# Kernel tuning notes

Measured on AMD Instinct MI355X. Metric: run time of the kernel, lower is better.

## Reference

```python
import jax, jax.numpy as jnp
import numpy as np

V = 32000   # vocab_size
HD = 512    # num_hiddens
B = 32      # batch
T = 128     # seq_len


def setup_inputs() -> dict:
    key = jax.random.key(0)
    ks = jax.random.split(key, 11)
    s_in = 1.0 / np.sqrt(V + HD)   # torch Linear default init bound
    s_out = 1.0 / np.sqrt(HD)

    def lin_w(k, out_f, in_f, s):
        return jax.random.uniform(k, (out_f, in_f), jnp.float32, -s, s)

    def lin_b(k, out_f, s):
        return jax.random.uniform(k, (out_f,), jnp.float32, -s, s)

    return {
        "X": jax.random.randint(ks[0], (B, T), 0, V),
        "H": jnp.zeros((B, HD), jnp.float32),
        "C": jnp.zeros((B, HD), jnp.float32),
        "Wf": lin_w(ks[1], HD, V + HD, s_in), "bf": lin_b(ks[2], HD, s_in),
        "Wi": lin_w(ks[3], HD, V + HD, s_in), "bi": lin_b(ks[4], HD, s_in),
        "Wo": lin_w(ks[5], HD, V + HD, s_in), "bo": lin_b(ks[6], HD, s_in),
        "Wc": lin_w(ks[7], HD, V + HD, s_in), "bc": lin_b(ks[8], HD, s_in),
        "Wy": lin_w(ks[9], V, HD, s_out),     "by": lin_b(ks[10], V, s_out),
    }


def reference(X, H, C, Wf, bf, Wi, bi, Wo, bo, Wc, bc, Wy, by):
    # X: [B, T] int tokens. Transposed to time-major like torch's X.T.
    Xt = X.T  # [T, B]
    hd = H.shape[1]
    v = Wf.shape[1] - hd

    def split(W):
        return W[:, :v], W[:, v:]  # input part, hidden part

    Wfx, Wfh = split(Wf)
    Wix, Wih = split(Wi)
    Wox, Woh = split(Wo)
    Wcx, Wch = split(Wc)

    # one_hot(x) @ Wx^T == row-gather of Wx^T: same math, no wasted compute.
    Ef = jnp.take(Wfx.T, Xt, axis=0) + bf  # [T, B, HD]
    Ei = jnp.take(Wix.T, Xt, axis=0) + bi
    Eo = jnp.take(Wox.T, Xt, axis=0) + bo
    Ec = jnp.take(Wcx.T, Xt, axis=0) + bc

    def step(carry, e):
        h, c = carry
        ef, ei, eo, ec = e
        f = jax.nn.sigmoid(ef + h @ Wfh.T)
        i = jax.nn.sigmoid(ei + h @ Wih.T)
        o = jax.nn.sigmoid(eo + h @ Woh.T)
        c_tilde = jnp.tanh(ec + h @ Wch.T)
        c = f * c + i * c_tilde
        h = o * jnp.tanh(c)
        return (h, c), h

    (H, C), Hs = jax.lax.scan(step, (H, C), (Ef, Ei, Eo, Ec))  # Hs: [T, B, HD]

    # per-step Y = h2out(H), then torch.cat(outputs, dim=0) -> [T*B, V]
    Y = Hs.reshape(-1, hd) @ Wy.T + by
    return Y, (H, C)
```

## Files before the change

### kernel.cpp

```cpp
#include <hip/hip_runtime.h>
#include <hip/hip_bf16.h>

#define V  32000
#define HD 512
#define BB 32
#define TT 128
#define VH 32512
#define LBLK 8
#define NBLK 256
#define GBLK (NBLK - LBLK)
#define NTILE (32 * 125)

typedef short  short8  __attribute__((ext_vector_type(8)));
typedef unsigned short u16x8 __attribute__((ext_vector_type(8)));
typedef unsigned short u16x4 __attribute__((ext_vector_type(4)));
typedef float  f32x4   __attribute__((ext_vector_type(4)));

__device__ __forceinline__ unsigned short bf16_rne(float f) {
  unsigned u = __builtin_bit_cast(unsigned, f);
  u += 0x7FFFu + ((u >> 16) & 1u);
  return (unsigned short)(u >> 16);
}

__device__ __forceinline__ void gload_lds16(const void* g, void* l) {
  __builtin_amdgcn_global_load_lds((const __attribute__((address_space(1))) void*)g,
                                   (__attribute__((address_space(3))) void*)l, 16, 0, 0);
}

__device__ __forceinline__ float sigf(float x) {
  return 1.0f / (1.0f + __expf(-x));
}
__device__ __forceinline__ float tanhf_fast(float x) {
  return 1.0f - 2.0f / (1.0f + __expf(2.0f * x));
}

__global__ void __launch_bounds__(512, 2) fused_all(
    const int* __restrict__ X,
    const float* __restrict__ Hin,
    const float* __restrict__ Cin,
    const float* __restrict__ Wf, const float* __restrict__ bfp,
    const float* __restrict__ Wi, const float* __restrict__ bip,
    const float* __restrict__ Wo, const float* __restrict__ bop,
    const float* __restrict__ Wc, const float* __restrict__ bcp,
    const float* __restrict__ Wy, const float* __restrict__ by,
    float* __restrict__ E,
    unsigned short* __restrict__ HsM1,
    unsigned short* __restrict__ Wyb,
    float* __restrict__ outHC,
    unsigned* __restrict__ bar,
    unsigned* __restrict__ bar2,
    unsigned* __restrict__ gcount,
    unsigned* __restrict__ wbar,
    float* __restrict__ Y)
{
  __shared__ __align__(16) char smem[75776];

  const int tid = threadIdx.x;
  const int blkid = blockIdx.x;
  const int wid = tid >> 6, lane = tid & 63;
  const int fr = lane & 15, ko = lane >> 4;

  unsigned short* Hs = HsM1 + BB * HD;

  if (blkid < LBLK) {
    short* hl = (short*)smem;
    float (*Pl)[BB][68] = (float(*)[BB][68])(smem + 32768);
    float (*cl)[64]     = (float(*)[64])(smem + 32768 + 34816);

    const int blk = blkid;
    const int g = wid & 3, qg = wid >> 2;

    const float* Wg = (g == 0) ? Wf : (g == 1) ? Wi : (g == 2) ? Wo : Wc;
    short8 wreg[2][16];
    #pragma unroll
    for (int n = 0; n < 2; ++n) {
      const int q = blk * 64 + qg * 32 + n * 16 + fr;
      const float* rowp = Wg + (size_t)q * VH + V;
      #pragma unroll
      for (int kk = 0; kk < 16; ++kk) {
        const float4 lo = *(const float4*)(rowp + kk * 32 + ko * 8);
        const float4 hi = *(const float4*)(rowp + kk * 32 + ko * 8 + 4);
        short8 w;
        w[0] = (short)bf16_rne(lo.x); w[1] = (short)bf16_rne(lo.y);
        w[2] = (short)bf16_rne(lo.z); w[3] = (short)bf16_rne(lo.w);
        w[4] = (short)bf16_rne(hi.x); w[5] = (short)bf16_rne(hi.y);
        w[6] = (short)bf16_rne(hi.z); w[7] = (short)bf16_rne(hi.w);
        wreg[n][kk] = w;
      }
    }

    const int e0 = tid * 4;
    const int eb = e0 >> 6, ql = e0 & 63;
    const int qglob = blk * 64 + ql;
    {
      const f32x4 c4 = *(const f32x4*)(Cin + eb * HD + qglob);
      *(f32x4*)&cl[eb][ql] = c4;
      const f32x4 h4 = *(const f32x4*)(Hin + eb * HD + qglob);
      u16x4 hq;
      #pragma unroll
      for (int j = 0; j < 4; ++j) hq[j] = bf16_rne(h4[j]);
      *(u16x4*)(HsM1 + (size_t)eb * HD + qglob) = hq;
    }
    __syncthreads();

    if (tid == 0) {
      __threadfence();
      __hip_atomic_fetch_add(bar, 1u, __ATOMIC_RELAXED, __HIP_MEMORY_SCOPE_AGENT);
      while (__hip_atomic_load(bar, __ATOMIC_RELAXED, __HIP_MEMORY_SCOPE_AGENT) < (unsigned)LBLK ||
             __hip_atomic_load(gcount, __ATOMIC_RELAXED, __HIP_MEMORY_SCOPE_AGENT) < (unsigned)TT) {}
      __threadfence();
    }
    __syncthreads();

    int abase[2], asw[2];
    #pragma unroll
    for (int m = 0; m < 2; ++m) {
      const int r = m * 16 + fr;
      abase[m] = r * 1024;
      asw[m] = (r & 7) << 4;
    }

    for (int t = 0; t < TT; ++t) {
      const float* Eb = E + ((size_t)t * 4) * BB * HD;
      const f32x4 ef = *(const f32x4*)(Eb + (size_t)(0 * BB + eb) * HD + qglob);
      const f32x4 ei = *(const f32x4*)(Eb + (size_t)(1 * BB + eb) * HD + qglob);
      const f32x4 eo = *(const f32x4*)(Eb + (size_t)(2 * BB + eb) * HD + qglob);
      const f32x4 ec = *(const f32x4*)(Eb + (size_t)(3 * BB + eb) * HD + qglob);

      if (t > 0) {
        __syncthreads();
        if (tid == 0) {
          __threadfence();
          __hip_atomic_fetch_add(bar, 1u, __ATOMIC_RELAXED, __HIP_MEMORY_SCOPE_AGENT);
          const unsigned tgt = (unsigned)(LBLK * (t + 1));
          while (__hip_atomic_load(bar, __ATOMIC_RELAXED, __HIP_MEMORY_SCOPE_AGENT) < tgt) {}
          __threadfence();
          if (blk == 0)
            __hip_atomic_store(bar2, (unsigned)t, __ATOMIC_RELAXED, __HIP_MEMORY_SCOPE_AGENT);
        }
        __syncthreads();
      }

      const char* hsrc = (const char*)(HsM1 + (size_t)t * (BB * HD));
      #pragma unroll
      for (int is = 0; is < 4; ++is) {
        const int i = is * 512 + tid;
        const int sb = (i >> 6) * 1024 + (((i & 63) * 16) ^ (((i >> 6) & 7) << 4));
        gload_lds16(hsrc + sb, (char*)hl + (size_t)(is * 512 + (tid & ~63)) * 16);
      }

      __syncthreads();

      f32x4 acc[2][2];
      #pragma unroll
      for (int m = 0; m < 2; ++m)
        #pragma unroll
        for (int n = 0; n < 2; ++n)
          acc[m][n] = (f32x4){0.f, 0.f, 0.f, 0.f};

      #pragma unroll
      for (int kk = 0; kk < 16; ++kk) {
        const int off = kk * 64 + ko * 16;
        const short8 a0 = *(const short8*)((const char*)hl + abase[0] + (off ^ asw[0]));
        const short8 a1 = *(const short8*)((const char*)hl + abase[1] + (off ^ asw[1]));
        acc[0][0] = __builtin_amdgcn_mfma_f32_16x16x32_bf16(a0, wreg[0][kk], acc[0][0], 0, 0, 0);
        acc[1][0] = __builtin_amdgcn_mfma_f32_16x16x32_bf16(a1, wreg[0][kk], acc[1][0], 0, 0, 0);
        acc[0][1] = __builtin_amdgcn_mfma_f32_16x16x32_bf16(a0, wreg[1][kk], acc[0][1], 0, 0, 0);
        acc[1][1] = __builtin_amdgcn_mfma_f32_16x16x32_bf16(a1, wreg[1][kk], acc[1][1], 0, 0, 0);
      }

      #pragma unroll
      for (int m = 0; m < 2; ++m)
        #pragma unroll
        for (int n = 0; n < 2; ++n)
          #pragma unroll
          for (int j = 0; j < 4; ++j)
            Pl[g][m * 16 + ko * 4 + j][qg * 32 + n * 16 + fr] = acc[m][n][j];
      __syncthreads();

      const f32x4 pf4 = *(const f32x4*)&Pl[0][eb][ql];
      const f32x4 pi4 = *(const f32x4*)&Pl[1][eb][ql];
      const f32x4 po4 = *(const f32x4*)&Pl[2][eb][ql];
      const f32x4 pc4 = *(const f32x4*)&Pl[3][eb][ql];
      const f32x4 cold = *(const f32x4*)&cl[eb][ql];
      f32x4 cnew, hnew;
      u16x4 hq;
      #pragma unroll
      for (int j = 0; j < 4; ++j) {
        const float fg = sigf(pf4[j] + ef[j]);
        const float ig = sigf(pi4[j] + ei[j]);
        const float og = sigf(po4[j] + eo[j]);
        const float ct = tanhf_fast(pc4[j] + ec[j]);
        const float cn = fg * cold[j] + ig * ct;
        const float hv = og * tanhf_fast(cn);
        cnew[j] = cn;
        hnew[j] = hv;
        hq[j] = bf16_rne(hv);
      }
      *(f32x4*)&cl[eb][ql] = cnew;
      *(u16x4*)(Hs + ((size_t)t * BB + eb) * HD + qglob) = hq;
      if (t == TT - 1) {
        *(f32x4*)(outHC + (size_t)eb * HD + qglob) = hnew;
        *(f32x4*)(outHC + (size_t)BB * HD + (size_t)eb * HD + qglob) = cnew;
      }
    }

    __syncthreads();
    if (tid == 0) {
      __threadfence();
      __hip_atomic_fetch_add(bar, 1u, __ATOMIC_RELAXED, __HIP_MEMORY_SCOPE_AGENT);
      if (blk == 0) {
        while (__hip_atomic_load(bar, __ATOMIC_RELAXED, __HIP_MEMORY_SCOPE_AGENT) < (unsigned)(LBLK * (TT + 1))) {}
        __threadfence();
        __hip_atomic_store(bar2, (unsigned)TT, __ATOMIC_RELAXED, __HIP_MEMORY_SCOPE_AGENT);
      }
    }
  } else {
    unsigned short* As = (unsigned short*)smem;
    unsigned short* Bs = (unsigned short*)(smem + 16384);
    int* xs            = (int*)(smem + 49152);

    const int tch = blkid - LBLK;
    if (tch < TT) {
      if (tid < BB) xs[tid] = X[tid * TT + tch];
      __syncthreads();
      const int q = tid;
      float* Erow = E + ((size_t)tch * 4) * BB * HD;
      #pragma unroll
      for (int g = 0; g < 4; ++g) {
        const float* W = (g == 0) ? Wf : (g == 1) ? Wi : (g == 2) ? Wo : Wc;
        const float* bsrc = (g == 0) ? bfp : (g == 1) ? bip : (g == 2) ? bop : bcp;
        const float bias = bsrc[q];
        const float* wq = W + (size_t)q * VH;
        #pragma unroll 4
        for (int b = 0; b < BB; ++b) {
          const float v = __builtin_nontemporal_load(wq + xs[b]);
          Erow[(size_t)(g * BB + b) * HD + q] = v + bias;
        }
      }
      __syncthreads();
      if (tid == 0) {
        __threadfence();
        __hip_atomic_fetch_add(gcount, 1u, __ATOMIC_RELAXED, __HIP_MEMORY_SCOPE_AGENT);
      }
    }

    {
      const size_t n = (size_t)V * HD;
      for (size_t i = ((size_t)(blkid - LBLK) * 512 + tid) * 8; i < n;
           i += (size_t)GBLK * 512 * 8) {
        const f32x4 a = __builtin_nontemporal_load((const f32x4*)(Wy + i));
        const f32x4 b = __builtin_nontemporal_load((const f32x4*)(Wy + i + 4));
        u16x8 o;
        o[0] = bf16_rne(a[0]); o[1] = bf16_rne(a[1]); o[2] = bf16_rne(a[2]); o[3] = bf16_rne(a[3]);
        o[4] = bf16_rne(b[0]); o[5] = bf16_rne(b[1]); o[6] = bf16_rne(b[2]); o[7] = bf16_rne(b[3]);
        *(u16x8*)(Wyb + i) = o;
      }
      __syncthreads();
      if (tid == 0) {
        __threadfence();
        __hip_atomic_fetch_add(wbar, 1u, __ATOMIC_RELAXED, __HIP_MEMORY_SCOPE_AGENT);
        while (__hip_atomic_load(wbar, __ATOMIC_RELAXED, __HIP_MEMORY_SCOPE_AGENT) < (unsigned)GBLK)
          __builtin_amdgcn_s_sleep(2);
        __threadfence();
      }
      __syncthreads();
    }

    const int wr = wid >> 2, wc = wid & 3;

    for (int tile = blkid - LBLK; tile < NTILE; tile += GBLK) {
      const int bm = tile / 125, bn = tile % 125;
      const int row0 = bm << 7, col0 = bn << 8;

      if (tid == 0) {
        const unsigned need = (unsigned)(4 * bm + 4);
        while (__hip_atomic_load(bar2, __ATOMIC_RELAXED, __HIP_MEMORY_SCOPE_AGENT) < need)
          __builtin_amdgcn_s_sleep(2);
        __threadfence();
      }
      __syncthreads();

      f32x4 acc[4][4];
      #pragma unroll
      for (int m = 0; m < 4; ++m)
        #pragma unroll
        for (int n = 0; n < 4; ++n)
          acc[m][n] = (f32x4){0.f, 0.f, 0.f, 0.f};

      for (int kt = 0; kt < 8; ++kt) {
        const int k0 = kt << 6;
        #pragma unroll
        for (int is = 0; is < 2; ++is) {
          const int id = is * 512 + tid;
          const int r = id >> 3;
          const int c = (id & 7) ^ (r & 7);
          gload_lds16(Hs + (size_t)(row0 + r) * 512 + k0 + c * 8,
                      &As[(is * 512 + (tid & ~63)) * 8]);
        }
        #pragma unroll
        for (int is = 0; is < 4; ++is) {
          const int id = is * 512 + tid;
          const int r = id >> 3;
          const int c = (id & 7) ^ (r & 7);
          gload_lds16(Wyb + (size_t)(col0 + r) * 512 + k0 + c * 8,
                      &Bs[(is * 512 + (tid & ~63)) * 8]);
        }
        __syncthreads();
        #pragma unroll
        for (int kk = 0; kk < 2; ++kk) {
          short8 af[4], bfr[4];
          #pragma unroll
          for (int m = 0; m < 4; ++m) {
            const int r = (wr << 6) + (m << 4) + fr;
            const int c = ((kk << 2) | ko) ^ (r & 7);
            af[m] = *(const short8*)&As[r * 64 + c * 8];
          }
          #pragma unroll
          for (int n = 0; n < 4; ++n) {
            const int r = (wc << 6) + (n << 4) + fr;
            const int c = ((kk << 2) | ko) ^ (r & 7);
            bfr[n] = *(const short8*)&Bs[r * 64 + c * 8];
          }
          #pragma unroll
          for (int m = 0; m < 4; ++m)
            #pragma unroll
            for (int n = 0; n < 4; ++n)
              acc[m][n] = __builtin_amdgcn_mfma_f32_16x16x32_bf16(
                  af[m], bfr[n], acc[m][n], 0, 0, 0);
        }
        __syncthreads();
      }

      const int rgrp = lane >> 4;
      #pragma unroll
      for (int n = 0; n < 4; ++n) {
        const int col = col0 + (wc << 6) + (n << 4) + fr;
        const float bias = by[col];
        #pragma unroll
        for (int m = 0; m < 4; ++m) {
          const int rowb = row0 + (wr << 6) + (m << 4) + (rgrp << 2);
          #pragma unroll
          for (int j = 0; j < 4; ++j) {
            __builtin_nontemporal_store(acc[m][n][j] + bias,
                                        &Y[(size_t)(rowb + j) * V + col]);
          }
        }
      }
    }
  }
}

extern "C" void kernel_launch(void* const* d_in, const int* in_sizes, int n_in,
                              void* d_out, int out_size, void* d_ws, size_t ws_size,
                              hipStream_t stream)
{
  const int*   X  = (const int*)  d_in[0];
  const float* H  = (const float*)d_in[1];
  const float* C  = (const float*)d_in[2];
  const float* Wf = (const float*)d_in[3];
  const float* bf = (const float*)d_in[4];
  const float* Wi = (const float*)d_in[5];
  const float* bi = (const float*)d_in[6];
  const float* Wo = (const float*)d_in[7];
  const float* bo = (const float*)d_in[8];
  const float* Wc = (const float*)d_in[9];
  const float* bc = (const float*)d_in[10];
  const float* Wy = (const float*)d_in[11];
  const float* by = (const float*)d_in[12];

  float* Y = (float*)d_out;
  float* outHC = Y + (size_t)TT * BB * V;

  char* ws = (char*)d_ws;
  float* E              = (float*)ws;
  unsigned short* Wyb   = (unsigned short*)(ws + 33554432);
  unsigned short* HsM1  = (unsigned short*)(ws + 66322432);
  unsigned* bar         = (unsigned*)(ws + 70549504);
  unsigned* bar2        = (unsigned*)(ws + 70549504 + 64);
  unsigned* gcount      = (unsigned*)(ws + 70549504 + 128);
  unsigned* wbar        = (unsigned*)(ws + 70549504 + 192);

  (void)hipMemsetAsync(bar, 0, 256, stream);

  {
    const int* X_p = X;
    const float *H_p = H, *C_p = C;
    const float *Wf_p = Wf, *bf_p = bf, *Wi_p = Wi, *bi_p = bi;
    const float *Wo_p = Wo, *bo_p = bo, *Wc_p = Wc, *bc_p = bc;
    const float *Wy_p = Wy, *by_p = by;
    float* E_p = E;
    unsigned short* HsM1_p = HsM1;
    unsigned short* Wyb_p = Wyb;
    float* outHC_p = outHC;
    unsigned *bar_p = bar, *bar2_p = bar2, *gcount_p = gcount, *wbar_p = wbar;
    float* Y_p = Y;
    void* args[] = {(void*)&X_p, (void*)&H_p, (void*)&C_p,
                    (void*)&Wf_p, (void*)&bf_p, (void*)&Wi_p, (void*)&bi_p,
                    (void*)&Wo_p, (void*)&bo_p, (void*)&Wc_p, (void*)&bc_p,
                    (void*)&Wy_p, (void*)&by_p,
                    (void*)&E_p, (void*)&HsM1_p, (void*)&Wyb_p, (void*)&outHC_p,
                    (void*)&bar_p, (void*)&bar2_p, (void*)&gcount_p, (void*)&wbar_p,
                    (void*)&Y_p};
    (void)hipLaunchCooperativeKernel((void*)fused_all, dim3(NBLK), dim3(512), args, 0, stream);
  }
}
```

Baseline: 1.048 ms.

## Enlarge output GEMM tiles, spread LSTM blocks, and add per-timestep embedding flags

```diff
diff --git a/kernel.cpp b/kernel.cpp
--- a/kernel.cpp
+++ b/kernel.cpp
@@ -9,7 +9,7 @@
 #define LBLK 8
 #define NBLK 256
 #define GBLK (NBLK - LBLK)
-#define NTILE (32 * 125)
+#define NTILE (16 * 125)
 
 typedef short  short8  __attribute__((ext_vector_type(8)));
 typedef unsigned short u16x8 __attribute__((ext_vector_type(8)));
@@ -34,7 +34,7 @@
   return 1.0f - 2.0f / (1.0f + __expf(2.0f * x));
 }
 
-__global__ void __launch_bounds__(512, 2) fused_all(
+__global__ void __launch_bounds__(512, 1) fused_all(
     const int* __restrict__ X,
     const float* __restrict__ Hin,
     const float* __restrict__ Cin,
@@ -49,8 +49,8 @@
     float* __restrict__ outHC,
     unsigned* __restrict__ bar,
     unsigned* __restrict__ bar2,
-    unsigned* __restrict__ gcount,
     unsigned* __restrict__ wbar,
+    unsigned* __restrict__ eflag,
     float* __restrict__ Y)
 {
   __shared__ __align__(16) char smem[75776];
@@ -62,12 +62,12 @@
 
   unsigned short* Hs = HsM1 + BB * HD;
 
-  if (blkid < LBLK) {
+  if (blkid < 64 && (blkid & 7) == 0) {
     short* hl = (short*)smem;
     float (*Pl)[BB][68] = (float(*)[BB][68])(smem + 32768);
     float (*cl)[64]     = (float(*)[64])(smem + 32768 + 34816);
 
-    const int blk = blkid;
+    const int blk = blkid >> 3;
     const int g = wid & 3, qg = wid >> 2;
 
     const float* Wg = (g == 0) ? Wf : (g == 1) ? Wi : (g == 2) ? Wo : Wc;
@@ -106,8 +106,8 @@
     if (tid == 0) {
       __threadfence();
       __hip_atomic_fetch_add(bar, 1u, __ATOMIC_RELAXED, __HIP_MEMORY_SCOPE_AGENT);
-      while (__hip_atomic_load(bar, __ATOMIC_RELAXED, __HIP_MEMORY_SCOPE_AGENT) < (unsigned)LBLK ||
-             __hip_atomic_load(gcount, __ATOMIC_RELAXED, __HIP_MEMORY_SCOPE_AGENT) < (unsigned)TT) {}
+      while (__hip_atomic_load(bar, __ATOMIC_RELAXED, __HIP_MEMORY_SCOPE_AGENT) < (unsigned)LBLK) {}
+      while (__hip_atomic_load(&eflag[0], __ATOMIC_RELAXED, __HIP_MEMORY_SCOPE_AGENT) < 2u) {}
       __threadfence();
     }
     __syncthreads();
@@ -121,33 +121,34 @@
     }
 
     for (int t = 0; t < TT; ++t) {
+      if (t > 0) {
+        __syncthreads();
+        if (tid == 0) {
+          __threadfence();
+          __hip_atomic_fetch_add(bar, 1u, __ATOMIC_RELAXED, __HIP_MEMORY_SCOPE_AGENT);
+          const unsigned tgt = (unsigned)(LBLK * (t + 1));
+          while (__hip_atomic_load(bar, __ATOMIC_RELAXED, __HIP_MEMORY_SCOPE_AGENT) < tgt) {}
+          while (__hip_atomic_load(&eflag[t], __ATOMIC_RELAXED, __HIP_MEMORY_SCOPE_AGENT) < 2u) {}
+          __threadfence();
+          if (blk == 0)
+            __hip_atomic_store(bar2, (unsigned)t, __ATOMIC_RELAXED, __HIP_MEMORY_SCOPE_AGENT);
+        }
+        __syncthreads();
+      }
+
+      const char* hsrc = (const char*)(HsM1 + (size_t)t * (BB * HD));
+      #pragma unroll
+      for (int is = 0; is < 4; ++is) {
+        const int i = is * 512 + tid;
+        const int sb = (i >> 6) * 1024 + (((i & 63) * 16) ^ (((i >> 6) & 7) << 4));
+        gload_lds16(hsrc + sb, (char*)hl + (size_t)(is * 512 + (tid & ~63)) * 16);
+      }
+
       const float* Eb = E + ((size_t)t * 4) * BB * HD;
       const f32x4 ef = *(const f32x4*)(Eb + (size_t)(0 * BB + eb) * HD + qglob);
       const f32x4 ei = *(const f32x4*)(Eb + (size_t)(1 * BB + eb) * HD + qglob);
       const f32x4 eo = *(const f32x4*)(Eb + (size_t)(2 * BB + eb) * HD + qglob);
       const f32x4 ec = *(const f32x4*)(Eb + (size_t)(3 * BB + eb) * HD + qglob);
-
-      if (t > 0) {
-        __syncthreads();
-        if (tid == 0) {
-          __threadfence();
-          __hip_atomic_fetch_add(bar, 1u, __ATOMIC_RELAXED, __HIP_MEMORY_SCOPE_AGENT);
-          const unsigned tgt = (unsigned)(LBLK * (t + 1));
-          while (__hip_atomic_load(bar, __ATOMIC_RELAXED, __HIP_MEMORY_SCOPE_AGENT) < tgt) {}
-          __threadfence();
-          if (blk == 0)
-            __hip_atomic_store(bar2, (unsigned)t, __ATOMIC_RELAXED, __HIP_MEMORY_SCOPE_AGENT);
-        }
-        __syncthreads();
-      }
-
-      const char* hsrc = (const char*)(HsM1 + (size_t)t * (BB * HD));
-      #pragma unroll
-      for (int is = 0; is < 4; ++is) {
-        const int i = is * 512 + tid;
-        const int sb = (i >> 6) * 1024 + (((i & 63) * 16) ^ (((i >> 6) & 7) << 4));
-        gload_lds16(hsrc + sb, (char*)hl + (size_t)(is * 512 + (tid & ~63)) * 16);
-      }
 
       __syncthreads();
 
@@ -217,37 +218,43 @@
     }
   } else {
     unsigned short* As = (unsigned short*)smem;
-    unsigned short* Bs = (unsigned short*)(smem + 16384);
-    int* xs            = (int*)(smem + 49152);
-
-    const int tch = blkid - LBLK;
-    if (tch < TT) {
-      if (tid < BB) xs[tid] = X[tid * TT + tch];
-      __syncthreads();
-      const int q = tid;
-      float* Erow = E + ((size_t)tch * 4) * BB * HD;
-      #pragma unroll
-      for (int g = 0; g < 4; ++g) {
-        const float* W = (g == 0) ? Wf : (g == 1) ? Wi : (g == 2) ? Wo : Wc;
-        const float* bsrc = (g == 0) ? bfp : (g == 1) ? bip : (g == 2) ? bop : bcp;
-        const float bias = bsrc[q];
-        const float* wq = W + (size_t)q * VH;
-        #pragma unroll 4
-        for (int b = 0; b < BB; ++b) {
-          const float v = __builtin_nontemporal_load(wq + xs[b]);
-          Erow[(size_t)(g * BB + b) * HD + q] = v + bias;
-        }
-      }
-      __syncthreads();
-      if (tid == 0) {
-        __threadfence();
-        __hip_atomic_fetch_add(gcount, 1u, __ATOMIC_RELAXED, __HIP_MEMORY_SCOPE_AGENT);
+    unsigned short* Bs = (unsigned short*)(smem + 32768);
+    int* xs            = (int*)(smem + 65536);
+
+    const int gid = (blkid < 64) ? (blkid - (blkid >> 3) - 1) : (blkid - 8);
+
+    #pragma unroll
+    for (int rep = 0; rep < 2; ++rep) {
+      const int u = gid + rep * GBLK;
+      if (u < 2 * TT) {
+        const int tg = u >> 1, half = u & 1;
+        if (tid < 16) xs[tid] = X[(half * 16 + tid) * TT + tg];
+        __syncthreads();
+        const int q = tid;
+        float* Erow = E + ((size_t)tg * 4) * BB * HD;
+        #pragma unroll
+        for (int g = 0; g < 4; ++g) {
+          const float* W = (g == 0) ? Wf : (g == 1) ? Wi : (g == 2) ? Wo : Wc;
+          const float* bsrc = (g == 0) ? bfp : (g == 1) ? bip : (g == 2) ? bop : bcp;
+          const float bias = bsrc[q];
+          const float* wq = W + (size_t)q * VH;
+          #pragma unroll 4
+          for (int b = 0; b < 16; ++b) {
+            const float v = __builtin_nontemporal_load(wq + xs[b]);
+            Erow[(size_t)(g * BB + half * 16 + b) * HD + q] = v + bias;
+          }
+        }
+        __syncthreads();
+        if (tid == 0) {
+          __threadfence();
+          __hip_atomic_fetch_add(&eflag[tg], 1u, __ATOMIC_RELAXED, __HIP_MEMORY_SCOPE_AGENT);
+        }
       }
     }
 
     {
       const size_t n = (size_t)V * HD;
-      for (size_t i = ((size_t)(blkid - LBLK) * 512 + tid) * 8; i < n;
+      for (size_t i = ((size_t)gid * 512 + tid) * 8; i < n;
            i += (size_t)GBLK * 512 * 8) {
         const f32x4 a = __builtin_nontemporal_load((const f32x4*)(Wy + i));
         const f32x4 b = __builtin_nontemporal_load((const f32x4*)(Wy + i + 4));
@@ -269,21 +276,21 @@
 
     const int wr = wid >> 2, wc = wid & 3;
 
-    for (int tile = blkid - LBLK; tile < NTILE; tile += GBLK) {
+    for (int tile = gid; tile < NTILE; tile += GBLK) {
       const int bm = tile / 125, bn = tile % 125;
-      const int row0 = bm << 7, col0 = bn << 8;
+      const int row0 = bm << 8, col0 = bn << 8;
 
       if (tid == 0) {
-        const unsigned need = (unsigned)(4 * bm + 4);
+        const unsigned need = (unsigned)(8 * bm + 8);
         while (__hip_atomic_load(bar2, __ATOMIC_RELAXED, __HIP_MEMORY_SCOPE_AGENT) < need)
           __builtin_amdgcn_s_sleep(2);
         __threadfence();
       }
       __syncthreads();
 
-      f32x4 acc[4][4];
-      #pragma unroll
-      for (int m = 0; m < 4; ++m)
+      f32x4 acc[8][4];
+      #pragma unroll
+      for (int m = 0; m < 8; ++m)
         #pragma unroll
         for (int n = 0; n < 4; ++n)
           acc[m][n] = (f32x4){0.f, 0.f, 0.f, 0.f};
@@ -291,7 +298,7 @@
       for (int kt = 0; kt < 8; ++kt) {
         const int k0 = kt << 6;
         #pragma unroll
-        for (int is = 0; is < 2; ++is) {
+        for (int is = 0; is < 4; ++is) {
           const int id = is * 512 + tid;
           const int r = id >> 3;
           const int c = (id & 7) ^ (r & 7);
@@ -309,21 +316,20 @@
         __syncthreads();
         #pragma unroll
         for (int kk = 0; kk < 2; ++kk) {
-          short8 af[4], bfr[4];
+          const int K = (kk << 2) | ko;
+          short8 af[8], bfr[4];
           #pragma unroll
-          for (int m = 0; m < 4; ++m) {
-            const int r = (wr << 6) + (m << 4) + fr;
-            const int c = ((kk << 2) | ko) ^ (r & 7);
-            af[m] = *(const short8*)&As[r * 64 + c * 8];
+          for (int m = 0; m < 8; ++m) {
+            const int r = (wr << 7) + (m << 4) + fr;
+            af[m] = *(const short8*)((const char*)As + r * 128 + ((K ^ (r & 7)) << 4));
           }
           #pragma unroll
           for (int n = 0; n < 4; ++n) {
             const int r = (wc << 6) + (n << 4) + fr;
-            const int c = ((kk << 2) | ko) ^ (r & 7);
-            bfr[n] = *(const short8*)&Bs[r * 64 + c * 8];
+            bfr[n] = *(const short8*)((const char*)Bs + r * 128 + ((K ^ (r & 7)) << 4));
           }
           #pragma unroll
-          for (int m = 0; m < 4; ++m)
+          for (int m = 0; m < 8; ++m)
             #pragma unroll
             for (int n = 0; n < 4; ++n)
               acc[m][n] = __builtin_amdgcn_mfma_f32_16x16x32_bf16(
@@ -338,8 +344,8 @@
         const int col = col0 + (wc << 6) + (n << 4) + fr;
         const float bias = by[col];
         #pragma unroll
-        for (int m = 0; m < 4; ++m) {
-          const int rowb = row0 + (wr << 6) + (m << 4) + (rgrp << 2);
+        for (int m = 0; m < 8; ++m) {
+          const int rowb = row0 + (wr << 7) + (m << 4) + (rgrp << 2);
           #pragma unroll
           for (int j = 0; j < 4; ++j) {
             __builtin_nontemporal_store(acc[m][n][j] + bias,
@@ -378,10 +384,10 @@
   unsigned short* HsM1  = (unsigned short*)(ws + 66322432);
   unsigned* bar         = (unsigned*)(ws + 70549504);
   unsigned* bar2        = (unsigned*)(ws + 70549504 + 64);
-  unsigned* gcount      = (unsigned*)(ws + 70549504 + 128);
-  unsigned* wbar        = (unsigned*)(ws + 70549504 + 192);
-
-  (void)hipMemsetAsync(bar, 0, 256, stream);
+  unsigned* wbar        = (unsigned*)(ws + 70549504 + 128);
+  unsigned* eflag       = (unsigned*)(ws + 70549504 + 256);
+
+  (void)hipMemsetAsync(bar, 0, 1024, stream);
 
   {
     const int* X_p = X;
@@ -393,14 +399,14 @@
     unsigned short* HsM1_p = HsM1;
     unsigned short* Wyb_p = Wyb;
     float* outHC_p = outHC;
-    unsigned *bar_p = bar, *bar2_p = bar2, *gcount_p = gcount, *wbar_p = wbar;
+    unsigned *bar_p = bar, *bar2_p = bar2, *wbar_p = wbar, *eflag_p = eflag;
     float* Y_p = Y;
     void* args[] = {(void*)&X_p, (void*)&H_p, (void*)&C_p,
                     (void*)&Wf_p, (void*)&bf_p, (void*)&Wi_p, (void*)&bi_p,
                     (void*)&Wo_p, (void*)&bo_p, (void*)&Wc_p, (void*)&bc_p,
                     (void*)&Wy_p, (void*)&by_p,
                     (void*)&E_p, (void*)&HsM1_p, (void*)&Wyb_p, (void*)&outHC_p,
-                    (void*)&bar_p, (void*)&bar2_p, (void*)&gcount_p, (void*)&wbar_p,
+                    (void*)&bar_p, (void*)&bar2_p, (void*)&wbar_p, (void*)&eflag_p,
                     (void*)&Y_p};
     (void)hipLaunchCooperativeKernel((void*)fused_all, dim3(NBLK), dim3(512), args, 0, stream);
   }
```

After: 1.216 ms. 1.16x slower.

## Place recurrence blocks on one XCD and relax per-step barrier synchronisation

Applied to the files above, without the earlier changes.

```diff
diff --git a/kernel.cpp b/kernel.cpp
--- a/kernel.cpp
+++ b/kernel.cpp
@@ -32,6 +32,16 @@
 }
 __device__ __forceinline__ float tanhf_fast(float x) {
   return 1.0f - 2.0f / (1.0f + __expf(2.0f * x));
+}
+
+__device__ __forceinline__ unsigned aload(const unsigned* p) {
+  return __hip_atomic_load(p, __ATOMIC_RELAXED, __HIP_MEMORY_SCOPE_AGENT);
+}
+__device__ __forceinline__ void astore(unsigned* p, unsigned v) {
+  __hip_atomic_store(p, v, __ATOMIC_RELAXED, __HIP_MEMORY_SCOPE_AGENT);
+}
+__device__ __forceinline__ unsigned aadd(unsigned* p, unsigned v) {
+  return __hip_atomic_fetch_add(p, v, __ATOMIC_RELAXED, __HIP_MEMORY_SCOPE_AGENT);
 }
 
 __global__ void __launch_bounds__(512, 2) fused_all(
@@ -49,25 +59,44 @@
     float* __restrict__ outHC,
     unsigned* __restrict__ bar,
     unsigned* __restrict__ bar2,
-    unsigned* __restrict__ gcount,
     unsigned* __restrict__ wbar,
+    unsigned* __restrict__ eflag,
+    unsigned* __restrict__ lticket,
+    unsigned* __restrict__ gticket,
     float* __restrict__ Y)
 {
   __shared__ __align__(16) char smem[75776];
+  __shared__ int sh_role;
 
   const int tid = threadIdx.x;
-  const int blkid = blockIdx.x;
   const int wid = tid >> 6, lane = tid & 63;
   const int fr = lane & 15, ko = lane >> 4;
 
   unsigned short* Hs = HsM1 + BB * HD;
 
-  if (blkid < LBLK) {
+  if (tid == 0) {
+    unsigned xcd;
+    asm volatile("s_getreg_b32 %0, hwreg(20, 0, 32)" : "=s"(xcd));
+    int role = -1;
+    if (xcd == 0) {
+      const unsigned s = aadd(lticket, 1u);
+      if (s < (unsigned)LBLK) role = (int)s;
+    }
+    if (role < 0) {
+      const unsigned g = aadd(gticket, 1u);
+      role = -(int)g - 2;
+    }
+    sh_role = role;
+  }
+  __syncthreads();
+  const int role = sh_role;
+
+  if (role >= 0) {
     short* hl = (short*)smem;
     float (*Pl)[BB][68] = (float(*)[BB][68])(smem + 32768);
     float (*cl)[64]     = (float(*)[64])(smem + 32768 + 34816);
 
-    const int blk = blkid;
+    const int blk = role;
     const int g = wid & 3, qg = wid >> 2;
 
     const float* Wg = (g == 0) ? Wf : (g == 1) ? Wi : (g == 2) ? Wo : Wc;
@@ -104,11 +133,9 @@
     __syncthreads();
 
     if (tid == 0) {
-      __threadfence();
-      __hip_atomic_fetch_add(bar, 1u, __ATOMIC_RELAXED, __HIP_MEMORY_SCOPE_AGENT);
-      while (__hip_atomic_load(bar, __ATOMIC_RELAXED, __HIP_MEMORY_SCOPE_AGENT) < (unsigned)LBLK ||
-             __hip_atomic_load(gcount, __ATOMIC_RELAXED, __HIP_MEMORY_SCOPE_AGENT) < (unsigned)TT) {}
-      __threadfence();
+      aadd(bar, 1u);
+      while (aload(bar) < (unsigned)LBLK) {}
+      while (aload(&eflag[0]) < 1u) {}
     }
     __syncthreads();
 
@@ -121,33 +148,34 @@
     }
 
     for (int t = 0; t < TT; ++t) {
+      if (t > 0) {
+        __syncthreads();
+        if (tid == 0) {
+          aadd(bar, 1u);
+          const unsigned tgt = (unsigned)(LBLK * (t + 1));
+          while (aload(bar) < tgt) {}
+          while (aload(&eflag[t]) < 1u) {}
+          if (blk == 0 && (t & 7) == 0) {
+            __threadfence();
+            astore(bar2, (unsigned)t);
+          }
+        }
+        __syncthreads();
+      }
+
+      const char* hsrc = (const char*)(HsM1 + (size_t)t * (BB * HD));
+      #pragma unroll
+      for (int is = 0; is < 4; ++is) {
+        const int i = is * 512 + tid;
+        const int sb = (i >> 6) * 1024 + (((i & 63) * 16) ^ (((i >> 6) & 7) << 4));
+        gload_lds16(hsrc + sb, (char*)hl + (size_t)(is * 512 + (tid & ~63)) * 16);
+      }
+
       const float* Eb = E + ((size_t)t * 4) * BB * HD;
       const f32x4 ef = *(const f32x4*)(Eb + (size_t)(0 * BB + eb) * HD + qglob);
       const f32x4 ei = *(const f32x4*)(Eb + (size_t)(1 * BB + eb) * HD + qglob);
       const f32x4 eo = *(const f32x4*)(Eb + (size_t)(2 * BB + eb) * HD + qglob);
       const f32x4 ec = *(const f32x4*)(Eb + (size_t)(3 * BB + eb) * HD + qglob);
-
-      if (t > 0) {
-        __syncthreads();
-        if (tid == 0) {
-          __threadfence();
-          __hip_atomic_fetch_add(bar, 1u, __ATOMIC_RELAXED, __HIP_MEMORY_SCOPE_AGENT);
-          const unsigned tgt = (unsigned)(LBLK * (t + 1));
-          while (__hip_atomic_load(bar, __ATOMIC_RELAXED, __HIP_MEMORY_SCOPE_AGENT) < tgt) {}
-          __threadfence();
-          if (blk == 0)
-            __hip_atomic_store(bar2, (unsigned)t, __ATOMIC_RELAXED, __HIP_MEMORY_SCOPE_AGENT);
-        }
-        __syncthreads();
-      }
-
-      const char* hsrc = (const char*)(HsM1 + (size_t)t * (BB * HD));
-      #pragma unroll
-      for (int is = 0; is < 4; ++is) {
-        const int i = is * 512 + tid;
-        const int sb = (i >> 6) * 1024 + (((i & 63) * 16) ^ (((i >> 6) & 7) << 4));
-        gload_lds16(hsrc + sb, (char*)hl + (size_t)(is * 512 + (tid & ~63)) * 16);
-      }
 
       __syncthreads();
 
@@ -207,12 +235,11 @@
 
     __syncthreads();
     if (tid == 0) {
-      __threadfence();
-      __hip_atomic_fetch_add(bar, 1u, __ATOMIC_RELAXED, __HIP_MEMORY_SCOPE_AGENT);
+      aadd(bar, 1u);
       if (blk == 0) {
-        while (__hip_atomic_load(bar, __ATOMIC_RELAXED, __HIP_MEMORY_SCOPE_AGENT) < (unsigned)(LBLK * (TT + 1))) {}
+        while (aload(bar) < (unsigned)(LBLK * (TT + 1))) {}
         __threadfence();
-        __hip_atomic_store(bar2, (unsigned)TT, __ATOMIC_RELAXED, __HIP_MEMORY_SCOPE_AGENT);
+        astore(bar2, (unsigned)TT);
       }
     }
   } else {
@@ -220,8 +247,10 @@
     unsigned short* Bs = (unsigned short*)(smem + 16384);
     int* xs            = (int*)(smem + 49152);
 
-    const int tch = blkid - LBLK;
-    if (tch < TT) {
+    const int gid = -role - 2;
+
+    if (gid < TT) {
+      const int tch = gid;
       if (tid < BB) xs[tid] = X[tid * TT + tch];
       __syncthreads();
       const int q = tid;
@@ -241,13 +270,13 @@
       __syncthreads();
       if (tid == 0) {
         __threadfence();
-        __hip_atomic_fetch_add(gcount, 1u, __ATOMIC_RELAXED, __HIP_MEMORY_SCOPE_AGENT);
+        astore(&eflag[tch], 1u);
       }
     }
 
     {
       const size_t n = (size_t)V * HD;
-      for (size_t i = ((size_t)(blkid - LBLK) * 512 + tid) * 8; i < n;
+      for (size_t i = ((size_t)gid * 512 + tid) * 8; i < n;
            i += (size_t)GBLK * 512 * 8) {
         const f32x4 a = __builtin_nontemporal_load((const f32x4*)(Wy + i));
         const f32x4 b = __builtin_nontemporal_load((const f32x4*)(Wy + i + 4));
@@ -259,25 +288,23 @@
       __syncthreads();
       if (tid == 0) {
         __threadfence();
-        __hip_atomic_fetch_add(wbar, 1u, __ATOMIC_RELAXED, __HIP_MEMORY_SCOPE_AGENT);
-        while (__hip_atomic_load(wbar, __ATOMIC_RELAXED, __HIP_MEMORY_SCOPE_AGENT) < (unsigned)GBLK)
+        aadd(wbar, 1u);
+        while (aload(wbar) < (unsigned)GBLK)
           __builtin_amdgcn_s_sleep(2);
-        __threadfence();
       }
       __syncthreads();
     }
 
     const int wr = wid >> 2, wc = wid & 3;
 
-    for (int tile = blkid - LBLK; tile < NTILE; tile += GBLK) {
+    for (int tile = gid; tile < NTILE; tile += GBLK) {
       const int bm = tile / 125, bn = tile % 125;
       const int row0 = bm << 7, col0 = bn << 8;
 
       if (tid == 0) {
         const unsigned need = (unsigned)(4 * bm + 4);
-        while (__hip_atomic_load(bar2, __ATOMIC_RELAXED, __HIP_MEMORY_SCOPE_AGENT) < need)
+        while (aload(bar2) < need)
           __builtin_amdgcn_s_sleep(2);
-        __threadfence();
       }
       __syncthreads();
 
@@ -378,10 +405,12 @@
   unsigned short* HsM1  = (unsigned short*)(ws + 66322432);
   unsigned* bar         = (unsigned*)(ws + 70549504);
   unsigned* bar2        = (unsigned*)(ws + 70549504 + 64);
-  unsigned* gcount      = (unsigned*)(ws + 70549504 + 128);
-  unsigned* wbar        = (unsigned*)(ws + 70549504 + 192);
-
-  (void)hipMemsetAsync(bar, 0, 256, stream);
+  unsigned* wbar        = (unsigned*)(ws + 70549504 + 128);
+  unsigned* lticket     = (unsigned*)(ws + 70549504 + 192);
+  unsigned* gticket     = (unsigned*)(ws + 70549504 + 256);
+  unsigned* eflag       = (unsigned*)(ws + 70549504 + 320);
+
+  (void)hipMemsetAsync(bar, 0, 1024, stream);
 
   {
     const int* X_p = X;
@@ -393,14 +422,16 @@
     unsigned short* HsM1_p = HsM1;
     unsigned short* Wyb_p = Wyb;
     float* outHC_p = outHC;
-    unsigned *bar_p = bar, *bar2_p = bar2, *gcount_p = gcount, *wbar_p = wbar;
+    unsigned *bar_p = bar, *bar2_p = bar2, *wbar_p = wbar, *eflag_p = eflag;
+    unsigned *lticket_p = lticket, *gticket_p = gticket;
     float* Y_p = Y;
     void* args[] = {(void*)&X_p, (void*)&H_p, (void*)&C_p,
                     (void*)&Wf_p, (void*)&bf_p, (void*)&Wi_p, (void*)&bi_p,
                     (void*)&Wo_p, (void*)&bo_p, (void*)&Wc_p, (void*)&bc_p,
                     (void*)&Wy_p, (void*)&by_p,
                     (void*)&E_p, (void*)&HsM1_p, (void*)&Wyb_p, (void*)&outHC_p,
-                    (void*)&bar_p, (void*)&bar2_p, (void*)&gcount_p, (void*)&wbar_p,
+                    (void*)&bar_p, (void*)&bar2_p, (void*)&wbar_p, (void*)&eflag_p,
+                    (void*)&lticket_p, (void*)&gticket_p,
                     (void*)&Y_p};
     (void)hipLaunchCooperativeKernel((void*)fused_all, dim3(NBLK), dim3(512), args, 0, stream);
   }
```

Result: faster. 900.3 us (-14.1%).
